# Performance work log

Measured on AMD Instinct MI355X. Metric: run time of the kernel, lower is better.

The kernel has to match this reference:

```python
import jax, jax.numpy as jnp
import numpy as np

B, C, H, S, DC = 32768, 1024, 1024, 8, 64  # batch, num_classes, hidden_dim, num_styles, calibrator dim

def setup_inputs() -> dict:
    key = jax.random.key(0)
    ks = jax.random.split(key, 12)
    inp = {
        "logits": jax.random.normal(ks[0], (B, C), dtype=jnp.float32),
        "style_idx": jax.random.randint(ks[1], (B,), 0, S, dtype=jnp.int32),
        # learned params
        "style_emb": jax.random.normal(ks[2], (S, H), dtype=jnp.float32),
        "Wa1": jax.random.normal(ks[3], (C + H, H), dtype=jnp.float32) * (1.0 / np.sqrt(C + H)),
        "ba1": jnp.zeros((H,), dtype=jnp.float32),
        "Wa2": jax.random.normal(ks[4], (H, C), dtype=jnp.float32) * (1.0 / np.sqrt(H)),
        "ba2": jnp.zeros((C,), dtype=jnp.float32),
        # per-style confidence calibrators: Linear(C,64) -> ReLU -> Linear(64,1) -> Sigmoid
        "Wc1": jax.random.normal(ks[5], (S, C, DC), dtype=jnp.float32) * (1.0 / np.sqrt(C)),
        "bc1": jnp.zeros((S, DC), dtype=jnp.float32),
        "Wc2": jax.random.normal(ks[6], (S, DC), dtype=jnp.float32) * (1.0 / np.sqrt(DC)),
        "bc2": jnp.zeros((S,), dtype=jnp.float32),
    }
    return inp

def reference(logits, style_idx, style_emb, Wa1, ba1, Wa2, ba2, Wc1, bc1, Wc2, bc2):
    # style embedding lookup + adapter MLP (residual on logits)
    emb = style_emb[style_idx]                                  # (B, H)
    combined = jnp.concatenate([logits, emb], axis=1)           # (B, C+H)
    hidden = jax.nn.relu(combined @ Wa1 + ba1)                  # (B, H)
    adjusted_logits = logits + hidden @ Wa2 + ba2               # (B, C)
    probs = jax.nn.softmax(adjusted_logits, axis=1)             # (B, C)
    # expert-routed confidence calibration: compute all styles densely, select per sample
    h = jax.nn.relu(jnp.einsum('bc,scd->bsd', probs, Wc1) + bc1)   # (B, S, DC)
    conf_all = jax.nn.sigmoid(jnp.einsum('bsd,sd->bs', h, Wc2) + bc2)  # (B, S)
    calibrated_confidence = jnp.take_along_axis(conf_all, style_idx[:, None].astype(jnp.int32), axis=1)  # (B, 1)
    return adjusted_logits, calibrated_confidence
```

## Files before the change

kernel.cpp:

```cpp
#include <hip/hip_runtime.h>
#include <hip/hip_bf16.h>
#include <stdint.h>

typedef __hip_bfloat16 bf16;
typedef __attribute__((ext_vector_type(8))) short short8;
typedef __attribute__((ext_vector_type(4))) float f32x4;

#define NB 32768
#define NC 1024
#define NH 1024
#define NS 8
#define NDC 64

__device__ __forceinline__ void gload_lds16(const void* g, void* l) {
    __builtin_amdgcn_global_load_lds((const __attribute__((address_space(1))) void*)g,
                                     (__attribute__((address_space(3))) void*)l, 16, 0, 0);
}

__device__ __forceinline__ short f2bf(float x) {
    bf16 h = __float2bfloat16(x);
    short s;
    __builtin_memcpy(&s, &h, 2);
    return s;
}

__global__ __launch_bounds__(256) void convert_kernel(
    const float* __restrict__ in, bf16* __restrict__ out)
{
    const size_t i = ((size_t)blockIdx.x * 256 + threadIdx.x) * 8;
    float4 a = *(const float4*)(in + i);
    float4 b = *(const float4*)(in + i + 4);
    short8 v;
    v[0] = f2bf(a.x); v[1] = f2bf(a.y); v[2] = f2bf(a.z); v[3] = f2bf(a.w);
    v[4] = f2bf(b.x); v[5] = f2bf(b.y); v[6] = f2bf(b.z); v[7] = f2bf(b.w);
    *(short8*)((short*)out + i) = v;
}

__global__ __launch_bounds__(256) void transpose_kernel(
    const float* __restrict__ in, bf16* __restrict__ out,
    int R, int Ccols, long long in_bs, long long out_bs)
{
    __shared__ float tile[32][33];
    const float* inb = in + (long long)blockIdx.z * in_bs;
    bf16* outb = out + (long long)blockIdx.z * out_bs;
    int c0 = blockIdx.x * 32, r0 = blockIdx.y * 32;
    int tx = threadIdx.x, ty = threadIdx.y;
#pragma unroll
    for (int i = 0; i < 32; i += 8)
        tile[ty + i][tx] = inb[(size_t)(r0 + ty + i) * Ccols + c0 + tx];
    __syncthreads();
#pragma unroll
    for (int i = 0; i < 32; i += 8)
        outb[(size_t)(c0 + ty + i) * R + r0 + tx] = __float2bfloat16(tile[tx][ty + i]);
}

__global__ __launch_bounds__(256) void style_partial_kernel(
    const float* __restrict__ style_emb, const float* __restrict__ Wa1,
    float* __restrict__ partial)
{
    const int h = (blockIdx.x & 3) * 256 + threadIdx.x;
    const int ks = blockIdx.x >> 2;
    float acc[NS];
#pragma unroll
    for (int s = 0; s < NS; ++s) acc[s] = 0.f;
#pragma unroll
    for (int kk = 0; kk < 16; ++kk) {
        const int k = ks * 16 + kk;
        const float w = Wa1[(size_t)(NC + k) * NH + h];
#pragma unroll
        for (int s = 0; s < NS; ++s)
            acc[s] += style_emb[s * NH + k] * w;
    }
#pragma unroll
    for (int s = 0; s < NS; ++s)
        partial[((size_t)ks * NS + s) * NH + h] = acc[s];
}

__global__ __launch_bounds__(256) void style_reduce_kernel(
    const float* __restrict__ partial, const float* __restrict__ ba1,
    float* __restrict__ out)
{
    const int i = blockIdx.x * 256 + threadIdx.x;
    const int h = i & (NH - 1);
    const int s = i >> 10;
    float acc = ba1[h];
#pragma unroll 8
    for (int ks = 0; ks < 64; ++ks)
        acc += partial[((size_t)ks * NS + s) * NH + h];
    out[i] = acc;
}

template<int MODE>
__global__ __launch_bounds__(256, 2) void gemm_kernel(
    const bf16* __restrict__ A, const bf16* __restrict__ BT,
    bf16* __restrict__ Cb, float* __restrict__ Cf,
    int N, int K,
    const float* __restrict__ style_contrib, const int* __restrict__ style_idx,
    const float* __restrict__ resid, const float* __restrict__ bias)
{
    __shared__ short lA[128 * 32];
    __shared__ short lB[128 * 32];

    const int t = threadIdx.x;
    const int lane = t & 63;
    const int wave = t >> 6;
    const int wr = wave >> 1;
    const int wc = wave & 1;

    const int nwg = gridDim.x * gridDim.y;
    const int flat = blockIdx.y * gridDim.x + blockIdx.x;
    const int cpx = nwg >> 3;
    const int swz = (flat & 7) * cpx + (flat >> 3);
    const int bm0 = (swz / gridDim.x) * 128;
    const int bn0 = (swz % gridDim.x) * 128;

    const int r0 = t >> 2;
    const int c8 = (t & 3) * 8;

    const int mrow = lane & 15;
    const int quad = lane >> 4;

    f32x4 acc[4][4];
#pragma unroll
    for (int i = 0; i < 4; ++i)
#pragma unroll
        for (int j = 0; j < 4; ++j) acc[i][j] = (f32x4){0.f, 0.f, 0.f, 0.f};

    const bf16* gA = A + (size_t)(bm0 + r0) * K + c8;
    const bf16* gB = BT + (size_t)(bn0 + r0) * K + c8;

    for (int k0 = 0; k0 < K; k0 += 32) {
        gload_lds16(gA + k0, lA + t * 8);
        gload_lds16(gA + (size_t)64 * K + k0, lA + 2048 + t * 8);
        gload_lds16(gB + k0, lB + t * 8);
        gload_lds16(gB + (size_t)64 * K + k0, lB + 2048 + t * 8);
        __syncthreads();

        short8 af[4], bfr[4];
#pragma unroll
        for (int i = 0; i < 4; ++i)
            af[i] = *(const short8*)(lA + (wr * 64 + i * 16 + mrow) * 32 + quad * 8);
#pragma unroll
        for (int j = 0; j < 4; ++j)
            bfr[j] = *(const short8*)(lB + (wc * 64 + j * 16 + mrow) * 32 + quad * 8);
#pragma unroll
        for (int i = 0; i < 4; ++i)
#pragma unroll
            for (int j = 0; j < 4; ++j)
                acc[i][j] = __builtin_amdgcn_mfma_f32_16x16x32_bf16(af[i], bfr[j], acc[i][j], 0, 0, 0);
        __syncthreads();
    }

#pragma unroll
    for (int i = 0; i < 4; ++i) {
#pragma unroll
        for (int r = 0; r < 4; ++r) {
            const int grow = bm0 + wr * 64 + i * 16 + quad * 4 + r;
            const float* scrow = nullptr;
            const float* resrow = nullptr;
            if (MODE == 0) scrow = style_contrib + (size_t)style_idx[grow] * N;
            if (MODE == 1) resrow = resid + (size_t)grow * N;
#pragma unroll
            for (int j = 0; j < 4; ++j) {
                const int gcol = bn0 + wc * 64 + j * 16 + mrow;
                float v = acc[i][j][r];
                if (MODE == 0) {
                    v += scrow[gcol];
                    v = fmaxf(v, 0.f);
                    Cb[(size_t)grow * N + gcol] = __float2bfloat16(v);
                } else {
                    v += resrow[gcol] + bias[gcol];
                    Cf[(size_t)grow * N + gcol] = v;
                }
            }
        }
    }
}

__global__ __launch_bounds__(256, 2) void gemm_conf_kernel(
    const bf16* __restrict__ A, const bf16* __restrict__ BT,
    int N, int K,
    const int* __restrict__ style_idx,
    const float* __restrict__ bc1, const float* __restrict__ Wc2,
    const float* __restrict__ bc2, float* __restrict__ conf_out)
{
    __shared__ short lA[128 * 32];
    __shared__ short lB[128 * 32];

    const int t = threadIdx.x;
    const int lane = t & 63;
    const int wave = t >> 6;
    const int wr = wave >> 1;
    const int wc = wave & 1;

    const int nwg = gridDim.x * gridDim.y;
    const int flat = blockIdx.y * gridDim.x + blockIdx.x;
    const int cpx = nwg >> 3;
    const int swz = (flat & 7) * cpx + (flat >> 3);
    const int bm0 = (swz / gridDim.x) * 128;
    const int bn0 = (swz % gridDim.x) * 128;

    const int r0 = t >> 2;
    const int c8 = (t & 3) * 8;

    const int mrow = lane & 15;
    const int quad = lane >> 4;

    f32x4 acc[4][4];
#pragma unroll
    for (int i = 0; i < 4; ++i)
#pragma unroll
        for (int j = 0; j < 4; ++j) acc[i][j] = (f32x4){0.f, 0.f, 0.f, 0.f};

    const bf16* gA = A + (size_t)(bm0 + r0) * K + c8;
    const bf16* gB = BT + (size_t)(bn0 + r0) * K + c8;

    for (int k0 = 0; k0 < K; k0 += 32) {
        gload_lds16(gA + k0, lA + t * 8);
        gload_lds16(gA + (size_t)64 * K + k0, lA + 2048 + t * 8);
        gload_lds16(gB + k0, lB + t * 8);
        gload_lds16(gB + (size_t)64 * K + k0, lB + 2048 + t * 8);
        __syncthreads();

        short8 af[4], bfr[4];
#pragma unroll
        for (int i = 0; i < 4; ++i)
            af[i] = *(const short8*)(lA + (wr * 64 + i * 16 + mrow) * 32 + quad * 8);
#pragma unroll
        for (int j = 0; j < 4; ++j)
            bfr[j] = *(const short8*)(lB + (wc * 64 + j * 16 + mrow) * 32 + quad * 8);
#pragma unroll
        for (int i = 0; i < 4; ++i)
#pragma unroll
            for (int j = 0; j < 4; ++j)
                acc[i][j] = __builtin_amdgcn_mfma_f32_16x16x32_bf16(af[i], bfr[j], acc[i][j], 0, 0, 0);
        __syncthreads();
    }

    const int s_w = (bn0 >> 6) + wc;
    float bcv[4], wcv[4];
#pragma unroll
    for (int j = 0; j < 4; ++j) {
        const int d = j * 16 + mrow;
        bcv[j] = bc1[s_w * NDC + d];
        wcv[j] = Wc2[s_w * NDC + d];
    }
    const float bias2 = bc2[s_w];

#pragma unroll
    for (int i = 0; i < 4; ++i) {
#pragma unroll
        for (int r = 0; r < 4; ++r) {
            const int grow = bm0 + wr * 64 + i * 16 + quad * 4 + r;
            float p = 0.f;
#pragma unroll
            for (int j = 0; j < 4; ++j)
                p += fmaxf(acc[i][j][r] + bcv[j], 0.f) * wcv[j];
#pragma unroll
            for (int off = 1; off < 16; off <<= 1) p += __shfl_xor(p, off, 64);
            if (mrow == 0 && style_idx[grow] == s_w)
                conf_out[grow] = 1.0f / (1.0f + __expf(-(p + bias2)));
        }
    }
}

__global__ __launch_bounds__(256) void softmax_kernel(
    const float* __restrict__ in, bf16* __restrict__ out)
{
    const size_t row = blockIdx.x;
    const float* x = in + row * NC;
    bf16* o = out + row * NC;
    const int t = threadIdx.x;
    __shared__ float red[8];

    float v[4];
    float m = -1e30f;
#pragma unroll
    for (int i = 0; i < 4; ++i) {
        v[i] = x[t + i * 256];
        m = fmaxf(m, v[i]);
    }
#pragma unroll
    for (int off = 1; off < 64; off <<= 1) m = fmaxf(m, __shfl_xor(m, off, 64));
    const int wv = t >> 6;
    if ((t & 63) == 0) red[wv] = m;
    __syncthreads();
    const float gm = fmaxf(fmaxf(red[0], red[1]), fmaxf(red[2], red[3]));

    float s = 0.f;
#pragma unroll
    for (int i = 0; i < 4; ++i) {
        v[i] = __expf(v[i] - gm);
        s += v[i];
    }
#pragma unroll
    for (int off = 1; off < 64; off <<= 1) s += __shfl_xor(s, off, 64);
    if ((t & 63) == 0) red[4 + wv] = s;
    __syncthreads();
    const float inv = 1.0f / (red[4] + red[5] + red[6] + red[7]);
#pragma unroll
    for (int i = 0; i < 4; ++i) o[t + i * 256] = __float2bfloat16(v[i] * inv);
}

extern "C" void kernel_launch(void* const* d_in, const int* in_sizes, int n_in,
                              void* d_out, int out_size, void* d_ws, size_t ws_size,
                              hipStream_t stream) {
    const float* logits    = (const float*)d_in[0];
    const int*   style_idx = (const int*)d_in[1];
    const float* style_emb = (const float*)d_in[2];
    const float* Wa1       = (const float*)d_in[3];
    const float* ba1       = (const float*)d_in[4];
    const float* Wa2       = (const float*)d_in[5];
    const float* ba2       = (const float*)d_in[6];
    const float* Wc1       = (const float*)d_in[7];
    const float* bc1       = (const float*)d_in[8];
    const float* Wc2       = (const float*)d_in[9];
    const float* bc2       = (const float*)d_in[10];

    char* ws = (char*)d_ws;
    bf16* logits_b = (bf16*)ws;        ws += (size_t)NB * NC * 2;
    bf16* hidden = (bf16*)ws;          ws += (size_t)NB * NH * 2;
    bf16* W1T = (bf16*)ws;             ws += (size_t)NC * NH * 2;
    bf16* W2T = (bf16*)ws;             ws += (size_t)NH * NC * 2;
    bf16* Wc1T = (bf16*)ws;            ws += (size_t)NS * NDC * NC * 2;
    float* style_contrib = (float*)ws; ws += (size_t)NS * NH * 4;
    float* style_partial = (float*)ws; ws += (size_t)64 * NS * NH * 4;

    float* adjusted = (float*)d_out;
    float* conf_out = (float*)d_out + (size_t)NB * NC;

    convert_kernel<<<(NB * NC) / (256 * 8), 256, 0, stream>>>(logits, logits_b);

    dim3 tb(32, 8);
    transpose_kernel<<<dim3(32, 32, 1), tb, 0, stream>>>(Wa1, W1T, NC, NH, 0, 0);
    transpose_kernel<<<dim3(32, 32, 1), tb, 0, stream>>>(Wa2, W2T, NH, NC, 0, 0);
    transpose_kernel<<<dim3(2, 32, NS), tb, 0, stream>>>(Wc1, Wc1T, NC, NDC,
                                                         (long long)NC * NDC, (long long)NDC * NC);
    style_partial_kernel<<<256, 256, 0, stream>>>(style_emb, Wa1, style_partial);
    style_reduce_kernel<<<NS * NH / 256, 256, 0, stream>>>(style_partial, ba1, style_contrib);

    gemm_kernel<0><<<dim3(NH / 128, NB / 128), 256, 0, stream>>>(
        logits_b, W1T, hidden, nullptr, NH, NC, style_contrib, style_idx, nullptr, nullptr);
    gemm_kernel<1><<<dim3(NC / 128, NB / 128), 256, 0, stream>>>(
        hidden, W2T, nullptr, adjusted, NC, NH, nullptr, nullptr, logits, ba2);
    softmax_kernel<<<NB, 256, 0, stream>>>(adjusted, hidden);
    gemm_conf_kernel<<<dim3((NS * NDC) / 128, NB / 128), 256, 0, stream>>>(
        hidden, Wc1T, NS * NDC, NC, style_idx, bc1, Wc2, bc2, conf_out);
}
```

Before: 528.0 us.

## Triple-buffer GEMM LDS loads with swizzled layout and merge conf kernel

Replaces the single-buffered GEMM main loop with a three-stage LDS ring. Loads for tile k+2 are issued before computing tile k, with vmcnt-based waits and one barrier per iteration, so global-to-LDS transfers overlap MFMA work. It also XOR-swizzles the LDS write and read positions to reduce bank conflicts, and folds the calibrator GEMM into the templated kernel as MODE 2. The cost is three times the LDS per block (48KB), which may limit occupancy against the launch bounds of 2 blocks per CU.

After: 540.5 us. +2.4%, slower.

```diff
diff --git a/kernel.cpp b/kernel.cpp
--- a/kernel.cpp
+++ b/kernel.cpp
@@ -96,10 +96,11 @@
     bf16* __restrict__ Cb, float* __restrict__ Cf,
     int N, int K,
     const float* __restrict__ style_contrib, const int* __restrict__ style_idx,
-    const float* __restrict__ resid, const float* __restrict__ bias)
-{
-    __shared__ short lA[128 * 32];
-    __shared__ short lB[128 * 32];
+    const float* __restrict__ resid, const float* __restrict__ bias,
+    const float* __restrict__ bc1, const float* __restrict__ Wc2,
+    const float* __restrict__ bc2, float* __restrict__ conf_out)
+{
+    __shared__ short lds[3 * 2 * 128 * 32];
 
     const int t = threadIdx.x;
     const int lane = t & 63;
@@ -114,11 +115,13 @@
     const int bm0 = (swz / gridDim.x) * 128;
     const int bn0 = (swz % gridDim.x) * 128;
 
-    const int r0 = t >> 2;
-    const int c8 = (t & 3) * 8;
+    const int tp = t ^ (((t >> 5) & 1) << 1);
+    const int r0 = tp >> 2;
+    const int c8 = (tp & 3) * 8;
 
     const int mrow = lane & 15;
     const int quad = lane >> 4;
+    const int qx8 = (quad ^ (((lane >> 3) & 1) << 1)) * 8;
 
     f32x4 acc[4][4];
 #pragma unroll
@@ -129,26 +132,74 @@
     const bf16* gA = A + (size_t)(bm0 + r0) * K + c8;
     const bf16* gB = BT + (size_t)(bn0 + r0) * K + c8;
 
-    for (int k0 = 0; k0 < K; k0 += 32) {
-        gload_lds16(gA + k0, lA + t * 8);
-        gload_lds16(gA + (size_t)64 * K + k0, lA + 2048 + t * 8);
-        gload_lds16(gB + k0, lB + t * 8);
-        gload_lds16(gB + (size_t)64 * K + k0, lB + 2048 + t * 8);
-        __syncthreads();
-
+    const int K32 = K >> 5;
+
+#define STAGE(kt, ob)                                                          \
+    do {                                                                       \
+        short* dst_ = lds + (ob);                                              \
+        gload_lds16(gA + (kt) * 32, dst_ + t * 8);                             \
+        gload_lds16(gA + (size_t)64 * K + (kt) * 32, dst_ + 2048 + t * 8);     \
+        gload_lds16(gB + (kt) * 32, dst_ + 4096 + t * 8);                      \
+        gload_lds16(gB + (size_t)64 * K + (kt) * 32, dst_ + 6144 + t * 8);     \
+    } while (0)
+
+    int ocur = 0, onxt = 8192, othr = 16384;
+    STAGE(0, ocur);
+    STAGE(1, onxt);
+
+    for (int kt = 0; kt < K32; ++kt) {
+        if (kt + 1 < K32)
+            asm volatile("s_waitcnt vmcnt(4)\n\ts_barrier" ::: "memory");
+        else
+            asm volatile("s_waitcnt vmcnt(0)\n\ts_barrier" ::: "memory");
+
+        if (kt + 2 < K32) STAGE(kt + 2, othr);
+
+        const short* pA = lds + ocur;
+        const short* pB = lds + ocur + 4096;
         short8 af[4], bfr[4];
 #pragma unroll
         for (int i = 0; i < 4; ++i)
-            af[i] = *(const short8*)(lA + (wr * 64 + i * 16 + mrow) * 32 + quad * 8);
+            af[i] = *(const short8*)(pA + (wr * 64 + i * 16 + mrow) * 32 + qx8);
 #pragma unroll
         for (int j = 0; j < 4; ++j)
-            bfr[j] = *(const short8*)(lB + (wc * 64 + j * 16 + mrow) * 32 + quad * 8);
+            bfr[j] = *(const short8*)(pB + (wc * 64 + j * 16 + mrow) * 32 + qx8);
 #pragma unroll
         for (int i = 0; i < 4; ++i)
 #pragma unroll
             for (int j = 0; j < 4; ++j)
                 acc[i][j] = __builtin_amdgcn_mfma_f32_16x16x32_bf16(af[i], bfr[j], acc[i][j], 0, 0, 0);
-        __syncthreads();
+
+        const int tmp = ocur; ocur = onxt; onxt = othr; othr = tmp;
+    }
+#undef STAGE
+
+    if (MODE == 2) {
+        const int s_w = (bn0 >> 6) + wc;
+        float bcv[4], wcv[4];
+#pragma unroll
+        for (int j = 0; j < 4; ++j) {
+            const int d = j * 16 + mrow;
+            bcv[j] = bc1[s_w * NDC + d];
+            wcv[j] = Wc2[s_w * NDC + d];
+        }
+        const float bias2 = bc2[s_w];
+#pragma unroll
+        for (int i = 0; i < 4; ++i) {
+#pragma unroll
+            for (int r = 0; r < 4; ++r) {
+                const int grow = bm0 + wr * 64 + i * 16 + quad * 4 + r;
+                float p = 0.f;
+#pragma unroll
+                for (int j = 0; j < 4; ++j)
+                    p += fmaxf(acc[i][j][r] + bcv[j], 0.f) * wcv[j];
+#pragma unroll
+                for (int off = 1; off < 16; off <<= 1) p += __shfl_xor(p, off, 64);
+                if (mrow == 0 && style_idx[grow] == s_w)
+                    conf_out[grow] = 1.0f / (1.0f + __expf(-(p + bias2)));
+            }
+        }
+        return;
     }
 
 #pragma unroll
@@ -173,93 +224,6 @@
                     Cf[(size_t)grow * N + gcol] = v;
                 }
             }
-        }
-    }
-}
-
-__global__ __launch_bounds__(256, 2) void gemm_conf_kernel(
-    const bf16* __restrict__ A, const bf16* __restrict__ BT,
-    int N, int K,
-    const int* __restrict__ style_idx,
-    const float* __restrict__ bc1, const float* __restrict__ Wc2,
-    const float* __restrict__ bc2, float* __restrict__ conf_out)
-{
-    __shared__ short lA[128 * 32];
-    __shared__ short lB[128 * 32];
-
-    const int t = threadIdx.x;
-    const int lane = t & 63;
-    const int wave = t >> 6;
-    const int wr = wave >> 1;
-    const int wc = wave & 1;
-
-    const int nwg = gridDim.x * gridDim.y;
-    const int flat = blockIdx.y * gridDim.x + blockIdx.x;
-    const int cpx = nwg >> 3;
-    const int swz = (flat & 7) * cpx + (flat >> 3);
-    const int bm0 = (swz / gridDim.x) * 128;
-    const int bn0 = (swz % gridDim.x) * 128;
-
-    const int r0 = t >> 2;
-    const int c8 = (t & 3) * 8;
-
-    const int mrow = lane & 15;
-    const int quad = lane >> 4;
-
-    f32x4 acc[4][4];
-#pragma unroll
-    for (int i = 0; i < 4; ++i)
-#pragma unroll
-        for (int j = 0; j < 4; ++j) acc[i][j] = (f32x4){0.f, 0.f, 0.f, 0.f};
-
-    const bf16* gA = A + (size_t)(bm0 + r0) * K + c8;
-    const bf16* gB = BT + (size_t)(bn0 + r0) * K + c8;
-
-    for (int k0 = 0; k0 < K; k0 += 32) {
-        gload_lds16(gA + k0, lA + t * 8);
-        gload_lds16(gA + (size_t)64 * K + k0, lA + 2048 + t * 8);
-        gload_lds16(gB + k0, lB + t * 8);
-        gload_lds16(gB + (size_t)64 * K + k0, lB + 2048 + t * 8);
-        __syncthreads();
-
-        short8 af[4], bfr[4];
-#pragma unroll
-        for (int i = 0; i < 4; ++i)
-            af[i] = *(const short8*)(lA + (wr * 64 + i * 16 + mrow) * 32 + quad * 8);
-#pragma unroll
-        for (int j = 0; j < 4; ++j)
-            bfr[j] = *(const short8*)(lB + (wc * 64 + j * 16 + mrow) * 32 + quad * 8);
-#pragma unroll
-        for (int i = 0; i < 4; ++i)
-#pragma unroll
-            for (int j = 0; j < 4; ++j)
-                acc[i][j] = __builtin_amdgcn_mfma_f32_16x16x32_bf16(af[i], bfr[j], acc[i][j], 0, 0, 0);
-        __syncthreads();
-    }
-
-    const int s_w = (bn0 >> 6) + wc;
-    float bcv[4], wcv[4];
-#pragma unroll
-    for (int j = 0; j < 4; ++j) {
-        const int d = j * 16 + mrow;
-        bcv[j] = bc1[s_w * NDC + d];
-        wcv[j] = Wc2[s_w * NDC + d];
-    }
-    const float bias2 = bc2[s_w];
-
-#pragma unroll
-    for (int i = 0; i < 4; ++i) {
-#pragma unroll
-        for (int r = 0; r < 4; ++r) {
-            const int grow = bm0 + wr * 64 + i * 16 + quad * 4 + r;
-            float p = 0.f;
-#pragma unroll
-            for (int j = 0; j < 4; ++j)
-                p += fmaxf(acc[i][j][r] + bcv[j], 0.f) * wcv[j];
-#pragma unroll
-            for (int off = 1; off < 16; off <<= 1) p += __shfl_xor(p, off, 64);
-            if (mrow == 0 && style_idx[grow] == s_w)
-                conf_out[grow] = 1.0f / (1.0f + __expf(-(p + bias2)));
         }
     }
 }
@@ -340,10 +304,13 @@
     style_reduce_kernel<<<NS * NH / 256, 256, 0, stream>>>(style_partial, ba1, style_contrib);
 
     gemm_kernel<0><<<dim3(NH / 128, NB / 128), 256, 0, stream>>>(
-        logits_b, W1T, hidden, nullptr, NH, NC, style_contrib, style_idx, nullptr, nullptr);
+        logits_b, W1T, hidden, nullptr, NH, NC, style_contrib, style_idx, nullptr, nullptr,
+        nullptr, nullptr, nullptr, nullptr);
     gemm_kernel<1><<<dim3(NC / 128, NB / 128), 256, 0, stream>>>(
-        hidden, W2T, nullptr, adjusted, NC, NH, nullptr, nullptr, logits, ba2);
+        hidden, W2T, nullptr, adjusted, NC, NH, nullptr, nullptr, logits, ba2,
+        nullptr, nullptr, nullptr, nullptr);
     softmax_kernel<<<NB, 256, 0, stream>>>(adjusted, hidden);
-    gemm_conf_kernel<<<dim3((NS * NDC) / 128, NB / 128), 256, 0, stream>>>(
-        hidden, Wc1T, NS * NDC, NC, style_idx, bc1, Wc2, bc2, conf_out);
-}
+    gemm_kernel<2><<<dim3((NS * NDC) / 128, NB / 128), 256, 0, stream>>>(
+        hidden, Wc1T, nullptr, nullptr, NS * NDC, NC, nullptr, style_idx, nullptr, nullptr,
+        bc1, Wc2, bc2, conf_out);
+}
```
